# Optimization experiments

Hardware: AMD Instinct MI355X
Metric: run time of the kernel (lower is better)

## Reference

```python
import jax, jax.numpy as jnp
import numpy as np

WS = 7          # window size (square)
HEADS = 16
LOGIT_MAX = float(np.log(1.0 / 0.01))


def _consts():
    # Continuous relative position bias coordinate table, Swin-v2 log-spaced.
    r = np.arange(-(WS - 1), WS)
    table = np.stack(np.meshgrid(r, r, indexing='ij'), axis=-1).astype(np.float32)  # [2W-1, 2W-1, 2]
    table = table / (WS - 1) * 8.0
    table = np.sign(table) * np.log2(np.abs(table) + 1.0) / np.log2(8.0)
    # Relative position index [N, N] into the flattened table.
    coords = np.stack(np.meshgrid(np.arange(WS), np.arange(WS), indexing='ij')).reshape(2, -1)
    rel = coords[:, :, None] - coords[:, None, :]
    idx = (rel[0] + WS - 1) * (2 * WS - 1) + (rel[1] + WS - 1)  # [49, 49]
    return table.reshape(-1, 2), idx.astype(np.int32)


def setup_inputs() -> dict:
    key = jax.random.key(0)
    ks = jax.random.split(key, 6)
    B, N, C = 2048, WS * WS, 512
    d = C // HEADS
    return {
        'x': jax.random.normal(ks[0], (B, N, C), jnp.float32),
        'w_qkv': jax.random.normal(ks[1], (C, 3 * C), jnp.float32) * (C ** -0.5),
        'q_bias': jnp.zeros((C,), jnp.float32),
        'v_bias': jnp.zeros((C,), jnp.float32),
        'logit_scale': jnp.full((HEADS, 1, 1), np.log(10.0), jnp.float32),
        'cpb_w1': jax.random.normal(ks[2], (2, 512), jnp.float32) * (2 ** -0.5),
        'cpb_b1': jnp.zeros((512,), jnp.float32),
        'cpb_w2': jax.random.normal(ks[3], (512, HEADS), jnp.float32) * (512 ** -0.5),
        'proj_w': jax.random.normal(ks[4], (C, C), jnp.float32) * (C ** -0.5),
        'proj_b': jnp.zeros((C,), jnp.float32),
    }


def _l2norm(x):
    # matches tf.math.l2_normalize (eps=1e-12 under a max)
    return x / jnp.sqrt(jnp.maximum(jnp.sum(x * x, axis=-1, keepdims=True), 1e-12))


def reference(x, w_qkv, q_bias, v_bias, logit_scale, cpb_w1, cpb_b1, cpb_w2, proj_w, proj_b):
    table, idx = _consts()
    table = jnp.asarray(table)   # [(2W-1)^2, 2]
    idx = jnp.asarray(idx)       # [N, N] int32 (constant)

    B, N, C = x.shape
    d = C // HEADS

    qkv = (x @ w_qkv).reshape(B, N, 3, HEADS, d).transpose(2, 0, 3, 1, 4)  # [3, B, H, N, d]
    q, k, v = qkv[0], qkv[1], qkv[2]
    q = q + q_bias.reshape(HEADS, 1, d)
    v = v + v_bias.reshape(HEADS, 1, d)

    # cosine attention with clamped learned logit scale
    attn = jnp.einsum('bhnd,bhmd->bhnm', _l2norm(q), _l2norm(k))
    scale = jnp.exp(jnp.minimum(logit_scale, LOGIT_MAX))  # [H,1,1]
    attn = attn * scale[None]

    # CPB MLP -> gather -> sigmoid bias
    bias_table = jax.nn.relu(table @ cpb_w1 + cpb_b1) @ cpb_w2          # [(2W-1)^2, H]
    bias = bias_table[idx.reshape(-1)].reshape(N, N, HEADS).transpose(2, 0, 1)  # [H, N, N]
    bias = 16.0 * jax.nn.sigmoid(bias)

    attn = jax.nn.softmax(attn + bias[None], axis=-1)

    out = jnp.einsum('bhnm,bhmd->bhnd', attn, v).transpose(0, 2, 1, 3).reshape(B, N, C)
    return out @ proj_w + proj_b
```

## Files before the change

kernel.cpp:

```cpp
#include <hip/hip_runtime.h>
#include <hip/hip_bf16.h>

typedef __bf16 bf16;
typedef __attribute__((ext_vector_type(8))) __bf16 bf16x8;
typedef __attribute__((ext_vector_type(4))) __bf16 bf16x4;
typedef __attribute__((ext_vector_type(4))) float floatx4;

#define HEADS 16
#define NTOK 49
#define MROWS (2048 * 49)
#define TILE_E 1568
#define LOGIT_MAX 4.6051702f


__device__ __forceinline__ void gload16(const void* g, void* l) {
  __builtin_amdgcn_global_load_lds((const __attribute__((address_space(1))) void*)g,
                                   (__attribute__((address_space(3))) void*)l, 16, 0, 0);
}


__global__ void cvt_x(const float* __restrict__ in, bf16* __restrict__ out, int n4) {
  int i = blockIdx.x * blockDim.x + threadIdx.x;
  const int stride = gridDim.x * blockDim.x;
  for (; i < n4; i += stride) {
    float4 v = ((const float4*)in)[i];
    bf16x4 o;
    o[0] = (bf16)v.x; o[1] = (bf16)v.y; o[2] = (bf16)v.z; o[3] = (bf16)v.w;
    *(bf16x4*)&out[(long)i * 4] = o;
  }
}

__global__ void transpose_bf16(const float* __restrict__ in, bf16* __restrict__ out,
                               int R, int C) {
  int idx = blockIdx.x * blockDim.x + threadIdx.x;
  if (idx < R * C) {
    int r = idx / C, c = idx % C;
    out[(long)c * R + r] = (bf16)in[(long)r * C + c];
  }
}


__global__ void cpb_mlp(const float* __restrict__ w1, const float* __restrict__ b1,
                        const float* __restrict__ w2, float* __restrict__ out169) {
  const int r = blockIdx.x;
  const int ti = r / 13, tj = r % 13;
  float v0 = (float)(ti - 6) * (8.0f / 6.0f);
  float v1 = (float)(tj - 6) * (8.0f / 6.0f);
  float s0 = (v0 > 0.f) ? 1.f : ((v0 < 0.f) ? -1.f : 0.f);
  float s1 = (v1 > 0.f) ? 1.f : ((v1 < 0.f) ? -1.f : 0.f);
  const float t0 = s0 * log2f(fabsf(v0) + 1.0f) * (1.0f / 3.0f);
  const float t1 = s1 * log2f(fabsf(v1) + 1.0f) * (1.0f / 3.0f);

  float acc[16];
#pragma unroll
  for (int h = 0; h < 16; ++h) acc[h] = 0.f;

  for (int c = threadIdx.x; c < 512; c += 64) {
    float hv = fmaxf(t0 * w1[c] + t1 * w1[512 + c] + b1[c], 0.f);
#pragma unroll
    for (int h = 0; h < 16; ++h) acc[h] += hv * w2[c * 16 + h];
  }
#pragma unroll
  for (int h = 0; h < 16; ++h) {
    float s = acc[h];
    for (int off = 32; off > 0; off >>= 1) s += __shfl_down(s, off);
    if (threadIdx.x == 0) out169[r * 16 + h] = s;
  }
}

__global__ void bias_expand(const float* __restrict__ out169, float* __restrict__ bias_sig) {
  int idx = blockIdx.x * blockDim.x + threadIdx.x;
  if (idx < 16 * 64 * 52) {
    int h = idx / 3328;
    int rem = idx % 3328;
    int q = rem / 52, k = rem % 52;
    float val = 0.f;
    if (q < 49 && k < 49) {
      int di = q / 7 - k / 7 + 6;
      int dj = q % 7 - k % 7 + 6;
      float v = out169[(di * 13 + dj) * 16 + h];
      val = 16.0f / (1.0f + expf(-v));
    }
    bias_sig[idx] = val;
  }
}


__device__ __forceinline__ void stage_tile(const bf16* __restrict__ G, int ldg,
                                           bf16* lds, int w, int lane) {
#pragma unroll
  for (int j = 0; j < 4; ++j) {
    const int rr = w * 32 + j * 8;
    const int row = rr + (lane >> 3);
    const int slot = (lane & 7) ^ (lane >> 3);
    gload16(G + (long)row * ldg + slot * 8, lds + rr * 64);
  }
}

template <int EPI>
__global__ __launch_bounds__(256, 4)
void gemm128(const bf16* __restrict__ A, const bf16* __restrict__ BT,
             void* __restrict__ Cout, const float* __restrict__ bias0,
             const float* __restrict__ bias1,
             bf16* __restrict__ Qp, bf16* __restrict__ Kp, bf16* __restrict__ Vp,
             int NT, int K, long N) {
  __shared__ bf16 AS[128][64];
  __shared__ bf16 BS[128][64];
  const int tid = threadIdx.x;
  const int lane = tid & 63, w = tid >> 6;
  const int l15 = lane & 15, g = lane >> 4;
  const int wm = w >> 1, wn = w & 1;

  int wg = blockIdx.x;
  wg = (wg & 7) * ((int)gridDim.x >> 3) + (wg >> 3);
  const long m0 = (long)(wg / NT) * 128;
  const long n0 = (long)(wg % NT) * 128;

  const bf16* Ab = A + m0 * K;
  const bf16* Bb = BT + n0 * K;

  floatx4 acc[4][4] = {};

  const int NKT = K >> 6;
  for (int kt = 0; kt < NKT; ++kt) {
    __syncthreads();
    stage_tile(Ab + kt * 64, K, &AS[0][0], w, lane);
    stage_tile(Bb + kt * 64, K, &BS[0][0], w, lane);
    __syncthreads();
#pragma unroll
    for (int t = 0; t < 2; ++t) {
      const int s = t * 4 + g;
      bf16x8 af[4], bfr[4];
#pragma unroll
      for (int m = 0; m < 4; ++m) {
        const int row = wm * 64 + m * 16 + l15;
        af[m] = *(const bf16x8*)&AS[row][(s ^ (row & 7)) * 8];
      }
#pragma unroll
      for (int n = 0; n < 4; ++n) {
        const int row = wn * 64 + n * 16 + l15;
        bfr[n] = *(const bf16x8*)&BS[row][(s ^ (row & 7)) * 8];
      }
#pragma unroll
      for (int m = 0; m < 4; ++m)
#pragma unroll
        for (int n = 0; n < 4; ++n)
          acc[m][n] = __builtin_amdgcn_mfma_f32_16x16x32_bf16(af[m], bfr[n], acc[m][n], 0, 0, 0);
    }
  }

  if (EPI == 0) {
    const int mat = (int)(n0 >> 9);
    bf16* const dst = (mat == 0) ? Qp : ((mat == 1) ? Kp : Vp);
    float badd4[4];
    unsigned off4[4];
#pragma unroll
    for (int n = 0; n < 4; ++n) {
      const int coln = (int)n0 + wn * 64 + n * 16;
      const int hh = (coln >> 5) & 15;
      const int d = (coln & 16) + l15;
      off4[n] = (unsigned)hh * TILE_E + d;
      badd4[n] = (mat == 0) ? bias0[coln + l15]
               : ((mat == 2) ? bias1[coln + l15 - 1024] : 0.0f);
    }
#pragma unroll
    for (int m = 0; m < 4; ++m) {
#pragma unroll
      for (int r = 0; r < 4; ++r) {
        const unsigned row = (unsigned)m0 + wm * 64 + m * 16 + g * 4 + r;
        const unsigned b = row / 49u;
        const unsigned nr = row - b * 49u;
        const unsigned ebase = b * (16u * TILE_E) + nr * 32u;
#pragma unroll
        for (int n = 0; n < 4; ++n)
          dst[ebase + off4[n]] = (bf16)(acc[m][n][r] + badd4[n]);
      }
    }
  } else {
#pragma unroll
    for (int m = 0; m < 4; ++m) {
#pragma unroll
      for (int n = 0; n < 4; ++n) {
        const long col = n0 + wn * 64 + n * 16 + l15;
        const float badd = bias0[col];
#pragma unroll
        for (int r = 0; r < 4; ++r) {
          const long row = m0 + wm * 64 + m * 16 + g * 4 + r;
          ((float*)Cout)[row * N + col] = acc[m][n][r] + badd;
        }
      }
    }
  }
}


__global__ __launch_bounds__(256)
void attn_mfma(const bf16* __restrict__ Qa, const bf16* __restrict__ Ka,
               const bf16* __restrict__ Va, const float* __restrict__ bias_sig,
               const float* __restrict__ logit_scale, bf16* __restrict__ aout) {
  __shared__ __align__(16) bf16 Vlds[4][2048];
  const int tid = threadIdx.x;
  const int wave = tid >> 6, lane = tid & 63;
  const int l15 = lane & 15, g = lane >> 4;
  const int bh = blockIdx.x * 4 + wave;
  const int h = bh & 15;
  const long tbase = (long)bh * TILE_E;
  const bf16* Qt = Qa + tbase;
  const bf16* Kt = Ka + tbase;
  const bf16* Vt = Va + tbase;
  bf16* VL = Vlds[wave];

#pragma unroll
  for (int j = 0; j < 4; ++j)
    gload16(Vt + j * 512 + lane * 8, VL + j * 512);

  bf16x8 kraw[4], qraw[4];
#pragma unroll
  for (int t = 0; t < 4; ++t)
    kraw[t] = *(const bf16x8*)(Kt + (t * 16 + l15) * 32 + g * 8);
#pragma unroll
  for (int t = 0; t < 4; ++t)
    qraw[t] = *(const bf16x8*)(Qt + (t * 16 + l15) * 32 + g * 8);

  const float scale = __expf(fminf(logit_scale[h], LOGIT_MAX));
  const float M = scale * 1.02f + 16.0f;

  bf16x8 kf[4], qf[4];
#pragma unroll
  for (int t = 0; t < 4; ++t) {
    float fv[8], ss = 0.f;
#pragma unroll
    for (int j = 0; j < 8; ++j) { fv[j] = (float)kraw[t][j]; ss += fv[j] * fv[j]; }
    ss += __shfl_xor(ss, 16);
    ss += __shfl_xor(ss, 32);
    const float rk = rsqrtf(fmaxf(ss, 1e-12f));
#pragma unroll
    for (int j = 0; j < 8; ++j) kf[t][j] = (bf16)(fv[j] * rk);
  }
#pragma unroll
  for (int t = 0; t < 4; ++t) {
    float fv[8], ss = 0.f;
#pragma unroll
    for (int j = 0; j < 8; ++j) { fv[j] = (float)qraw[t][j]; ss += fv[j] * fv[j]; }
    ss += __shfl_xor(ss, 16);
    ss += __shfl_xor(ss, 32);
    const float rq = rsqrtf(fmaxf(ss, 1e-12f));
#pragma unroll
    for (int j = 0; j < 8; ++j) qf[t][j] = (bf16)(fv[j] * rq);
  }

  asm volatile("s_waitcnt vmcnt(0)" ::: "memory");
  __builtin_amdgcn_sched_barrier(0);
  bf16x8 vf[2][2];
#pragma unroll
  for (int dt = 0; dt < 2; ++dt)
#pragma unroll
    for (int t = 0; t < 2; ++t)
#pragma unroll
      for (int i = 0; i < 8; ++i) {
        const int kk = t * 32 + (i >> 2) * 16 + g * 4 + (i & 3);
        vf[dt][t][i] = VL[kk * 32 + dt * 16 + l15];
      }

  const floatx4 zero = {};

#pragma unroll
  for (int qt = 0; qt < 4; ++qt) {
    const int qrow = qt * 16 + l15;

    float4 b4[4];
#pragma unroll
    for (int kt = 0; kt < 4; ++kt)
      b4[kt] = *(const float4*)(bias_sig + h * 3328 + qrow * 52 + kt * 16 + g * 4);

    floatx4 st[4];
#pragma unroll
    for (int kt = 0; kt < 4; ++kt)
      st[kt] = __builtin_amdgcn_mfma_f32_16x16x32_bf16(kf[kt], qf[qt], zero, 0, 0, 0);

    float sv[4][4];
    float l = 0.f;
#pragma unroll
    for (int kt = 0; kt < 4; ++kt)
#pragma unroll
      for (int r = 0; r < 4; ++r) {
        const int k = kt * 16 + g * 4 + r;
        const float s = (k < NTOK) ? st[kt][r] * scale + ((const float*)&b4[kt])[r] - M
                                   : -87.0f;
        const float p = __expf(s);
        sv[kt][r] = p;
        l += p;
      }
    l += __shfl_xor(l, 16);
    l += __shfl_xor(l, 32);
    const float inv = 1.0f / l;

    bf16x8 pa[2];
#pragma unroll
    for (int t = 0; t < 2; ++t)
#pragma unroll
      for (int i = 0; i < 8; ++i)
        pa[t][i] = (bf16)(sv[2 * t + (i >> 2)][i & 3] * inv);

    floatx4 ot[2] = {};
#pragma unroll
    for (int dt = 0; dt < 2; ++dt)
#pragma unroll
      for (int t = 0; t < 2; ++t)
        ot[dt] = __builtin_amdgcn_mfma_f32_16x16x32_bf16(pa[t], vf[dt][t], ot[dt], 0, 0, 0);

#pragma unroll
    for (int dt = 0; dt < 2; ++dt)
#pragma unroll
      for (int r = 0; r < 4; ++r) {
        const int q = qt * 16 + g * 4 + r;
        if (q < NTOK) VL[q * 40 + dt * 16 + l15] = (bf16)ot[dt][r];
      }
  }

  asm volatile("s_waitcnt lgkmcnt(0)" ::: "memory");
  __builtin_amdgcn_sched_barrier(0);
  const long obase = (long)(bh >> 4) * NTOK * 512 + h * 32;
#pragma unroll
  for (int j = 0; j < 4; ++j) {
    const int c = lane + 64 * j;
    if (c < 196) {
      const int row = c >> 2, part = c & 3;
      bf16x8 v = *(const bf16x8*)&VL[row * 40 + part * 8];
      *(bf16x8*)(aout + obase + (long)row * 512 + part * 8) = v;
    }
  }
}


extern "C" void kernel_launch(void* const* d_in, const int* in_sizes, int n_in,
                              void* d_out, int out_size, void* d_ws, size_t ws_size,
                              hipStream_t stream) {
  (void)in_sizes; (void)n_in; (void)out_size; (void)ws_size;
  const float* x           = (const float*)d_in[0];
  const float* w_qkv       = (const float*)d_in[1];
  const float* q_bias      = (const float*)d_in[2];
  const float* v_bias      = (const float*)d_in[3];
  const float* logit_scale = (const float*)d_in[4];
  const float* cpb_w1      = (const float*)d_in[5];
  const float* cpb_b1      = (const float*)d_in[6];
  const float* cpb_w2      = (const float*)d_in[7];
  const float* proj_w      = (const float*)d_in[8];
  const float* proj_b      = (const float*)d_in[9];
  float* out = (float*)d_out;

  char* ws = (char*)d_ws;
  const size_t ARR_B  = 102760448;
  const size_t WQT_B  = 1572864;
  const size_t PJT_B  = 524288;
  const size_t T169_B = 10816;
  bf16*  Qa       = (bf16*)ws;
  bf16*  Ka       = (bf16*)(ws + ARR_B);
  bf16*  Va       = (bf16*)(ws + 2 * ARR_B);
  bf16*  xbf      = (bf16*)(ws + 3 * ARR_B);
  bf16*  wqkvT    = (bf16*)(ws + 4 * ARR_B);
  bf16*  projT    = (bf16*)(ws + 4 * ARR_B + WQT_B);
  float* tab169   = (float*)(ws + 4 * ARR_B + WQT_B + PJT_B);
  float* bias_sig = (float*)(ws + 4 * ARR_B + WQT_B + PJT_B + T169_B);

  cvt_x<<<2048, 256, 0, stream>>>(x, xbf, MROWS * 512 / 4);
  transpose_bf16<<<3072, 256, 0, stream>>>(w_qkv, wqkvT, 512, 1536);
  transpose_bf16<<<1024, 256, 0, stream>>>(proj_w, projT, 512, 512);
  cpb_mlp<<<169, 64, 0, stream>>>(cpb_w1, cpb_b1, cpb_w2, tab169);
  bias_expand<<<208, 256, 0, stream>>>(tab169, bias_sig);

  gemm128<0><<<784 * 12, 256, 0, stream>>>(xbf, wqkvT, nullptr, q_bias, v_bias,
                                           Qa, Ka, Va, 12, 512, 1536);
  attn_mfma<<<8192, 256, 0, stream>>>(Qa, Ka, Va, bias_sig, logit_scale, xbf);
  gemm128<1><<<784 * 4, 256, 0, stream>>>(xbf, projT, out, proj_b, nullptr,
                                          nullptr, nullptr, nullptr, 4, 512, 512);
}
```

Measured before the change: 489.6 us.

## Fuse fp32-to-bf16 conversion of x into the QKV GEMM tile load

Drops the standalone cvt_x kernel. The QKV GEMM now stages fp32 x tiles straight into LDS with direct global-to-LDS loads, using a new swizzle, and converts them to bf16 while building MFMA fragments. This removes one full read and write pass over the 200MB activation. In exchange the GEMM reads fp32 A from global memory 12 times (once per N-tile), uses double the A-tile LDS, and runs at lower occupancy (launch bounds 3).

```diff
diff --git a/kernel.cpp b/kernel.cpp
--- a/kernel.cpp
+++ b/kernel.cpp
@@ -16,18 +16,6 @@
 __device__ __forceinline__ void gload16(const void* g, void* l) {
   __builtin_amdgcn_global_load_lds((const __attribute__((address_space(1))) void*)g,
                                    (__attribute__((address_space(3))) void*)l, 16, 0, 0);
-}
-
-
-__global__ void cvt_x(const float* __restrict__ in, bf16* __restrict__ out, int n4) {
-  int i = blockIdx.x * blockDim.x + threadIdx.x;
-  const int stride = gridDim.x * blockDim.x;
-  for (; i < n4; i += stride) {
-    float4 v = ((const float4*)in)[i];
-    bf16x4 o;
-    o[0] = (bf16)v.x; o[1] = (bf16)v.y; o[2] = (bf16)v.z; o[3] = (bf16)v.w;
-    *(bf16x4*)&out[(long)i * 4] = o;
-  }
 }
 
 __global__ void transpose_bf16(const float* __restrict__ in, bf16* __restrict__ out,
@@ -98,13 +86,13 @@
 }
 
 template <int EPI>
-__global__ __launch_bounds__(256, 4)
-void gemm128(const bf16* __restrict__ A, const bf16* __restrict__ BT,
+__global__ __launch_bounds__(256, EPI == 0 ? 3 : 4)
+void gemm128(const void* __restrict__ Ain, const bf16* __restrict__ BT,
              void* __restrict__ Cout, const float* __restrict__ bias0,
              const float* __restrict__ bias1,
              bf16* __restrict__ Qp, bf16* __restrict__ Kp, bf16* __restrict__ Vp,
              int NT, int K, long N) {
-  __shared__ bf16 AS[128][64];
+  __shared__ __align__(16) char ASraw[EPI == 0 ? 32768 : 16384];
   __shared__ bf16 BS[128][64];
   const int tid = threadIdx.x;
   const int lane = tid & 63, w = tid >> 6;
@@ -116,7 +104,8 @@
   const long m0 = (long)(wg / NT) * 128;
   const long n0 = (long)(wg % NT) * 128;
 
-  const bf16* Ab = A + m0 * K;
+  const float* Af = (const float*)Ain + m0 * K;
+  const bf16* Ab = (const bf16*)Ain + m0 * K;
   const bf16* Bb = BT + n0 * K;
 
   floatx4 acc[4][4] = {};
@@ -124,22 +113,52 @@
   const int NKT = K >> 6;
   for (int kt = 0; kt < NKT; ++kt) {
     __syncthreads();
-    stage_tile(Ab + kt * 64, K, &AS[0][0], w, lane);
+    if (EPI == 0) {
+#pragma unroll
+      for (int j = 0; j < 8; ++j) {
+        const int rr = w * 32 + j * 4;
+        const int row = rr + (lane >> 4);
+        const int slot = (lane & 15) ^ (row & 15);
+        gload16(Af + (long)row * K + kt * 64 + slot * 4, ASraw + rr * 256);
+      }
+    } else {
+      stage_tile(Ab + kt * 64, K, (bf16*)ASraw, w, lane);
+    }
     stage_tile(Bb + kt * 64, K, &BS[0][0], w, lane);
     __syncthreads();
 #pragma unroll
     for (int t = 0; t < 2; ++t) {
-      const int s = t * 4 + g;
       bf16x8 af[4], bfr[4];
-#pragma unroll
-      for (int m = 0; m < 4; ++m) {
-        const int row = wm * 64 + m * 16 + l15;
-        af[m] = *(const bf16x8*)&AS[row][(s ^ (row & 7)) * 8];
-      }
-#pragma unroll
-      for (int n = 0; n < 4; ++n) {
-        const int row = wn * 64 + n * 16 + l15;
-        bfr[n] = *(const bf16x8*)&BS[row][(s ^ (row & 7)) * 8];
+      if (EPI == 0) {
+        const float* ASf = (const float*)ASraw;
+        const int s2 = t * 8 + g * 2;
+#pragma unroll
+        for (int m = 0; m < 4; ++m) {
+          const int row = wm * 64 + m * 16 + l15;
+          const int rs = row & 15;
+          float4 lo = *(const float4*)&ASf[row * 64 + ((s2 ^ rs) * 4)];
+          float4 hi = *(const float4*)&ASf[row * 64 + (((s2 + 1) ^ rs) * 4)];
+          bf16x8 a;
+          a[0] = (bf16)lo.x; a[1] = (bf16)lo.y; a[2] = (bf16)lo.z; a[3] = (bf16)lo.w;
+          a[4] = (bf16)hi.x; a[5] = (bf16)hi.y; a[6] = (bf16)hi.z; a[7] = (bf16)hi.w;
+          af[m] = a;
+        }
+      } else {
+        const bf16* ASb = (const bf16*)ASraw;
+        const int s = t * 4 + g;
+#pragma unroll
+        for (int m = 0; m < 4; ++m) {
+          const int row = wm * 64 + m * 16 + l15;
+          af[m] = *(const bf16x8*)&ASb[row * 64 + ((s ^ (row & 7)) * 8)];
+        }
+      }
+      {
+        const int s = t * 4 + g;
+#pragma unroll
+        for (int n = 0; n < 4; ++n) {
+          const int row = wn * 64 + n * 16 + l15;
+          bfr[n] = *(const bf16x8*)&BS[row][(s ^ (row & 7)) * 8];
+        }
       }
 #pragma unroll
       for (int m = 0; m < 4; ++m)
@@ -363,13 +382,12 @@
   float* tab169   = (float*)(ws + 4 * ARR_B + WQT_B + PJT_B);
   float* bias_sig = (float*)(ws + 4 * ARR_B + WQT_B + PJT_B + T169_B);
 
-  cvt_x<<<2048, 256, 0, stream>>>(x, xbf, MROWS * 512 / 4);
   transpose_bf16<<<3072, 256, 0, stream>>>(w_qkv, wqkvT, 512, 1536);
   transpose_bf16<<<1024, 256, 0, stream>>>(proj_w, projT, 512, 512);
   cpb_mlp<<<169, 64, 0, stream>>>(cpb_w1, cpb_b1, cpb_w2, tab169);
   bias_expand<<<208, 256, 0, stream>>>(tab169, bias_sig);
 
-  gemm128<0><<<784 * 12, 256, 0, stream>>>(xbf, wqkvT, nullptr, q_bias, v_bias,
+  gemm128<0><<<784 * 12, 256, 0, stream>>>(x, wqkvT, nullptr, q_bias, v_bias,
                                            Qa, Ka, Va, 12, 512, 1536);
   attn_mfma<<<8192, 256, 0, stream>>>(Qa, Ka, Va, bias_sig, logit_scale, xbf);
   gemm128<1><<<784 * 4, 256, 0, stream>>>(xbf, projT, out, proj_b, nullptr,
```

Measured after the change: 490.9 us. About the same (+0.3%).
